# Optimization experiments

Measured on AMD Instinct MI355X. Metric: run time of the kernel, lower is better.

## Reference

```python
import jax, jax.numpy as jnp
import numpy as np

N_LAYERS = 2
NUM_BRANCHES = 3
TOPK_START = 10
TOPK_END = 3


def normalize_adj(adj):
    # symmetric degree normalization: D^-1/2 (A + I) D^-1/2
    n = adj.shape[0]
    a = jnp.clip(adj + jnp.eye(n, dtype=adj.dtype), 1e-8, jnp.inf)
    row_sum = jnp.clip(a.sum(axis=1), 1e-8, jnp.inf)
    d = jnp.clip(row_sum ** -0.5, 0.0, 100.0)
    return d[:, None] * a * d[None, :]


def setup_inputs() -> dict:
    key = jax.random.key(0)
    k1, k2 = jax.random.split(key)
    B, T, N, C = 512, 16, 22, 64
    x = jax.random.normal(k1, (B, T, N, C), dtype=jnp.float32)
    # emulate nn.Parameter init: clamp(adj,0,1)*0.01 + 0.05*I
    raw = jax.random.uniform(k2, (N, N), dtype=jnp.float32)
    adj = jnp.clip(raw, 0.0, 1.0) * 0.01 + 0.05 * jnp.eye(N, dtype=jnp.float32)
    branch_temps = jnp.ones((NUM_BRANCHES,), dtype=jnp.float32)
    fusion_logits = jnp.zeros((N_LAYERS, NUM_BRANCHES), dtype=jnp.float32)
    return {"x": x, "adj": adj, "branch_temps": branch_temps, "fusion_logits": fusion_logits}


def reference(x, adj, branch_temps, fusion_logits):
    B, T, N, C = x.shape
    # [B, T, N, C] -> [B, N, T*C]
    x0 = jnp.transpose(x, (0, 2, 1, 3)).reshape(B, N, T * C)
    A = normalize_adj(jnp.clip(adj, 0.0, 1.0))          # [N, N]
    temps = jnp.clip(branch_temps, 0.1, 10.0)           # [nb]
    eye = jnp.eye(N, dtype=x0.dtype)

    xb = x0
    for layer in range(N_LAYERS):
        K = int(TOPK_START - (TOPK_START - TOPK_END) * (layer / max(1, N_LAYERS - 1)))
        K = min(K, N)
        alpha = jax.nn.softmax(fusion_logits[layer])    # [nb]
        # cosine similarity, masked by normalized adjacency
        xn = xb / (jnp.linalg.norm(xb, axis=-1, keepdims=True) + 1e-6)
        sim = jnp.einsum('bnd,bmd->bnm', xn, xn) * A    # [B, N, N]
        # per-branch temperature + diagonal boost
        att = sim[None] / temps[:, None, None, None] + 0.1 * eye  # [nb, B, N, N]
        # annealed top-k sparsification (zeros still participate in softmax, as in torch)
        _, idx = jax.lax.top_k(att, K)                  # [nb, B, N, K]
        mask = jax.nn.one_hot(idx, N, dtype=att.dtype).sum(axis=-2)  # [nb, B, N, N]
        att = jax.nn.softmax(att * mask, axis=-1)
        y = jnp.einsum('kbnm,bmd->kbnd', att, xb)       # branch aggregation
        xb = jnp.einsum('k,kbnd->bnd', alpha, y)        # fusion
        if layer > 0:
            xb = xb + x0
        if layer < N_LAYERS - 1:
            xb = jax.nn.relu(xb)  # dropout identity in eval mode
    return xb, A
```

## Files before the change

kernel.cpp:

```cpp
#include <hip/hip_runtime.h>
#include <hip/hip_bf16.h>

#define BATCH  512
#define TT     16
#define NN     22
#define CC     64
#define DD     1024
#define NB     3
#define XS     1032
#define NTHR   512

typedef __bf16 bf16x8 __attribute__((ext_vector_type(8)));
typedef float  f32x4  __attribute__((ext_vector_type(4)));

__device__ __forceinline__ unsigned bf16rne(float x) {
  unsigned u = __float_as_uint(x);
  u += 0x7fffu + ((u >> 16) & 1u);
  return u >> 16;
}
__device__ __forceinline__ unsigned pack2(float a, float b) {
  return bf16rne(a) | (bf16rne(b) << 16);
}

__global__ __launch_bounds__(NTHR) void mbdsca_fused(
    const float* __restrict__ x,
    const float* __restrict__ adj,
    const float* __restrict__ btemps,
    const float* __restrict__ flogits,
    float* __restrict__ out)
{
  __shared__ unsigned short xs[NN][XS];
  __shared__ float As[NN][NN];
  __shared__ float Gs[NN][NN];
  __shared__ float Ws[NN][NN];
  __shared__ float attB[NB][NN][NN];
  __shared__ float norms[NN];
  __shared__ float alphas[2][NB];
  __shared__ float tvals[NB];

  const int tid = threadIdx.x;
  const int b   = blockIdx.x;
  const int lane = tid & 63;
  const int wv   = tid >> 6;

  if (tid < NN * NN) {
    int n = tid / NN, m = tid - n * NN;
    float v = adj[tid];
    v = fminf(fmaxf(v, 0.0f), 1.0f);
    if (n == m) v += 1.0f;
    v = fmaxf(v, 1e-8f);
    As[n][m] = v;
  }
  if (tid < NB) tvals[tid] = fminf(fmaxf(btemps[tid], 0.1f), 10.0f);
  __syncthreads();

  if (tid < NN) {
    float s = 0.0f;
    for (int m = 0; m < NN; ++m) s += As[tid][m];
    s = fmaxf(s, 1e-8f);
    norms[tid] = fminf(fmaxf(1.0f / sqrtf(s), 0.0f), 100.0f);
  }
  if (tid == 0) {
    for (int l = 0; l < 2; ++l) {
      float l0 = flogits[l*NB+0], l1 = flogits[l*NB+1], l2 = flogits[l*NB+2];
      float mx = fmaxf(l0, fmaxf(l1, l2));
      float e0 = __expf(l0-mx), e1 = __expf(l1-mx), e2 = __expf(l2-mx);
      float s = e0 + e1 + e2;
      alphas[l][0] = e0/s; alphas[l][1] = e1/s; alphas[l][2] = e2/s;
    }
  }
  __syncthreads();

  if (tid < NN * NN) {
    int n = tid / NN, m = tid - n * NN;
    As[n][m] = norms[n] * As[n][m] * norms[m];
  }
  #pragma unroll
  for (int j = 0; j < 11; ++j) {
    int f4  = tid + j * NTHR;
    int t   = f4 / (NN * (CC/4));
    int rem = f4 - t * (NN * (CC/4));
    int n   = rem >> 4;
    int c4  = rem & 15;
    const float4 v = *(const float4*)(&x[(size_t)b * (TT*NN*CC) + (size_t)f4 * 4]);
    uint2 p; p.x = pack2(v.x, v.y); p.y = pack2(v.z, v.w);
    *(uint2*)(&xs[n][t * CC + c4 * 4]) = p;
  }
  __syncthreads();

  for (int layer = 0; layer < 2; ++layer) {
    const int K = (layer == 0) ? 10 : 3;

    if (wv < 4) {
      const int Mt = wv >> 1, Nt = wv & 1;
      int arow = Mt * 16 + (lane & 15); if (arow > NN-1) arow = NN-1;
      int brow = Nt * 16 + (lane & 15); if (brow > NN-1) brow = NN-1;
      const int koff = (lane >> 4) * 8;
      f32x4 acc = {0.f, 0.f, 0.f, 0.f};
      #pragma unroll 4
      for (int ks = 0; ks < 32; ++ks) {
        bf16x8 a = *reinterpret_cast<const bf16x8*>(&xs[arow][ks * 32 + koff]);
        bf16x8 bb = *reinterpret_cast<const bf16x8*>(&xs[brow][ks * 32 + koff]);
        acc = __builtin_amdgcn_mfma_f32_16x16x32_bf16(a, bb, acc, 0, 0, 0);
      }
      #pragma unroll
      for (int r = 0; r < 4; ++r) {
        int row = Mt * 16 + (lane >> 4) * 4 + r;
        int col = Nt * 16 + (lane & 15);
        if (row < NN && col < NN) Gs[row][col] = acc[r];
      }
    }
    __syncthreads();

    if (tid < NN) norms[tid] = sqrtf(Gs[tid][tid]) + 1e-6f;
    __syncthreads();

    if (tid < NN * NN) {
      int n = tid / NN, m = tid - n * NN;
      Gs[n][m] = Gs[n][m] / (norms[n] * norms[m]) * As[n][m];
    }
    __syncthreads();

    for (int q = tid; q < NB * NN * NN; q += NTHR) {
      int k = q / (NN*NN), r = q - k * (NN*NN);
      int n = r / NN, m = r - n * NN;
      const float rtk = 1.0f / tvals[k];
      float v = Gs[n][m] * rtk + ((n == m) ? 0.1f : 0.0f);
      int rank = 0;
      #pragma unroll
      for (int j = 0; j < NN; ++j) {
        float vj = Gs[n][j] * rtk + ((n == j) ? 0.1f : 0.0f);
        rank += (vj > v) || (vj == v && j < m);
      }
      attB[k][n][m] = (rank < K) ? v : 0.0f;
    }
    __syncthreads();

    if (tid < NB * NN) {
      int k = tid / NN, n = tid - k * NN;
      float mx = -1e30f;
      for (int m = 0; m < NN; ++m) mx = fmaxf(mx, attB[k][n][m]);
      float s = 0.0f;
      for (int m = 0; m < NN; ++m) s += __expf(attB[k][n][m] - mx);
      float sc = alphas[layer][k] / s;
      for (int m = 0; m < NN; ++m) attB[k][n][m] = __expf(attB[k][n][m] - mx) * sc;
    }
    __syncthreads();

    if (tid < NN * NN) {
      int n = tid / NN, m = tid - n * NN;
      Ws[n][m] = attB[0][n][m] + attB[1][n][m] + attB[2][n][m];
    }
    __syncthreads();

    f32x4 acc[11];
    #pragma unroll
    for (int j = 0; j < 11; ++j) {
      const int g4 = tid + j * NTHR;
      const int n  = g4 >> 8;
      const int d4 = g4 & 255;
      f32x4 a = {0.f, 0.f, 0.f, 0.f};
      for (int m = 0; m < NN; ++m) {
        const float w = Ws[n][m];
        const uint2 u = *(const uint2*)(&xs[m][d4 * 4]);
        a[0] += w * __uint_as_float(u.x << 16);
        a[1] += w * __uint_as_float(u.x & 0xffff0000u);
        a[2] += w * __uint_as_float(u.y << 16);
        a[3] += w * __uint_as_float(u.y & 0xffff0000u);
      }
      acc[j] = a;
    }
    __syncthreads();

    if (layer == 0) {
      #pragma unroll
      for (int j = 0; j < 11; ++j) {
        const int g4 = tid + j * NTHR;
        const int n  = g4 >> 8;
        const int d4 = g4 & 255;
        f32x4 a = acc[j];
        uint2 p;
        p.x = pack2(fmaxf(a[0], 0.f), fmaxf(a[1], 0.f));
        p.y = pack2(fmaxf(a[2], 0.f), fmaxf(a[3], 0.f));
        *(uint2*)(&xs[n][d4 * 4]) = p;
      }
      __syncthreads();
    } else {
      #pragma unroll
      for (int j = 0; j < 11; ++j) {
        const int g4 = tid + j * NTHR;
        const int n  = g4 >> 8;
        const int d4 = g4 & 255;
        const float4 r = *(const float4*)(
            &x[(size_t)b * (TT*NN*CC) + (size_t)(d4 >> 4) * (NN*CC) + n * CC + (d4 & 15) * 4]);
        f32x4 a = acc[j];
        *(float4*)(&out[((size_t)b * NN + n) * DD + d4 * 4]) =
            make_float4(a[0] + r.x, a[1] + r.y, a[2] + r.z, a[3] + r.w);
      }
    }
  }

  if (b == 0 && tid < NN * NN) {
    out[(size_t)BATCH * NN * DD + tid] = As[tid / NN][tid - (tid / NN) * NN];
  }
}

extern "C" void kernel_launch(void* const* d_in, const int* in_sizes, int n_in,
                              void* d_out, int out_size, void* d_ws, size_t ws_size,
                              hipStream_t stream) {
  const float* x       = (const float*)d_in[0];
  const float* adj     = (const float*)d_in[1];
  const float* btemps  = (const float*)d_in[2];
  const float* flogits = (const float*)d_in[3];
  float* out = (float*)d_out;
  mbdsca_fused<<<BATCH, NTHR, 0, stream>>>(x, adj, btemps, flogits, out);
}
```

Before: 57.17 us.

## Move neighbor aggregation onto MFMA with hi/lo bf16 weights and split-K Gram

Replaces the per-thread scalar FMA aggregation over 22 neighbors with 16x16x32 bf16 MFMAs. The fused weight matrix is split into high and low bf16 parts so precision stays close to fp32. The Gram matrix now uses 32x32x16 MFMAs with a K-split across four waves, whose partial results are summed in shared memory. The softmax row max is computed inside the top-k rank loop, and the per-branch softmax is folded into the weight-fusion step, which removes a pass and a barrier. The trade-off is that the final output and residual accesses become scalar strided stores and loads rather than float4, and layer 0 updates xs in place per column tile.

```diff
diff --git a/kernel.cpp b/kernel.cpp
--- a/kernel.cpp
+++ b/kernel.cpp
@@ -9,9 +9,12 @@
 #define NB     3
 #define XS     1032
 #define NTHR   512
+#define WPAD   40
 
 typedef __bf16 bf16x8 __attribute__((ext_vector_type(8)));
 typedef float  f32x4  __attribute__((ext_vector_type(4)));
+typedef float  f32x16 __attribute__((ext_vector_type(16)));
+typedef short  s16x8  __attribute__((ext_vector_type(8)));
 
 __device__ __forceinline__ unsigned bf16rne(float x) {
   unsigned u = __float_as_uint(x);
@@ -31,15 +34,18 @@
 {
   __shared__ unsigned short xs[NN][XS];
   __shared__ float As[NN][NN];
-  __shared__ float Gs[NN][NN];
-  __shared__ float Ws[NN][NN];
+  __shared__ float Gp[4][NN][NN];
   __shared__ float attB[NB][NN][NN];
-  __shared__ float norms[NN];
+  __shared__ float mxs[NB][NN];
+  __shared__ float sinv[NB][NN];
+  __shared__ unsigned short Wh[32][WPAD];
+  __shared__ unsigned short Wl[32][WPAD];
+  __shared__ float dnorm[NN];
   __shared__ float alphas[2][NB];
   __shared__ float tvals[NB];
 
-  const int tid = threadIdx.x;
-  const int b   = blockIdx.x;
+  const int tid  = threadIdx.x;
+  const int b    = blockIdx.x;
   const int lane = tid & 63;
   const int wv   = tid >> 6;
 
@@ -48,17 +54,20 @@
     float v = adj[tid];
     v = fminf(fmaxf(v, 0.0f), 1.0f);
     if (n == m) v += 1.0f;
-    v = fmaxf(v, 1e-8f);
-    As[n][m] = v;
+    As[n][m] = fmaxf(v, 1e-8f);
   }
   if (tid < NB) tvals[tid] = fminf(fmaxf(btemps[tid], 0.1f), 10.0f);
+  for (int i = tid; i < 32 * WPAD / 2; i += NTHR) {
+    ((unsigned*)Wh)[i] = 0u;
+    ((unsigned*)Wl)[i] = 0u;
+  }
   __syncthreads();
 
   if (tid < NN) {
     float s = 0.0f;
     for (int m = 0; m < NN; ++m) s += As[tid][m];
     s = fmaxf(s, 1e-8f);
-    norms[tid] = fminf(fmaxf(1.0f / sqrtf(s), 0.0f), 100.0f);
+    dnorm[tid] = fminf(fmaxf(1.0f / sqrtf(s), 0.0f), 100.0f);
   }
   if (tid == 0) {
     for (int l = 0; l < 2; ++l) {
@@ -73,7 +82,7 @@
 
   if (tid < NN * NN) {
     int n = tid / NN, m = tid - n * NN;
-    As[n][m] = norms[n] * As[n][m] * norms[m];
+    As[n][m] = dnorm[n] * As[n][m] * dnorm[m];
   }
   #pragma unroll
   for (int j = 0; j < 11; ++j) {
@@ -92,32 +101,36 @@
     const int K = (layer == 0) ? 10 : 3;
 
     if (wv < 4) {
-      const int Mt = wv >> 1, Nt = wv & 1;
-      int arow = Mt * 16 + (lane & 15); if (arow > NN-1) arow = NN-1;
-      int brow = Nt * 16 + (lane & 15); if (brow > NN-1) brow = NN-1;
-      const int koff = (lane >> 4) * 8;
-      f32x4 acc = {0.f, 0.f, 0.f, 0.f};
-      #pragma unroll 4
-      for (int ks = 0; ks < 32; ++ks) {
-        bf16x8 a = *reinterpret_cast<const bf16x8*>(&xs[arow][ks * 32 + koff]);
-        bf16x8 bb = *reinterpret_cast<const bf16x8*>(&xs[brow][ks * 32 + koff]);
-        acc = __builtin_amdgcn_mfma_f32_16x16x32_bf16(a, bb, acc, 0, 0, 0);
-      }
-      #pragma unroll
-      for (int r = 0; r < 4; ++r) {
-        int row = Mt * 16 + (lane >> 4) * 4 + r;
-        int col = Nt * 16 + (lane & 15);
-        if (row < NN && col < NN) Gs[row][col] = acc[r];
-      }
-    }
-    __syncthreads();
-
-    if (tid < NN) norms[tid] = sqrtf(Gs[tid][tid]) + 1e-6f;
+      int row = lane & 31; if (row > NN-1) row = NN-1;
+      const int hi = lane >> 5;
+      f32x16 acc0 = {}, acc1 = {};
+      #pragma unroll
+      for (int s = 0; s < 16; ++s) {
+        int ks = wv * 16 + s;
+        bf16x8 a = *(const bf16x8*)(&xs[row][ks * 16 + hi * 8]);
+        if (s & 1) acc1 = __builtin_amdgcn_mfma_f32_32x32x16_bf16(a, a, acc1, 0, 0, 0);
+        else       acc0 = __builtin_amdgcn_mfma_f32_32x32x16_bf16(a, a, acc0, 0, 0, 0);
+      }
+      #pragma unroll
+      for (int r = 0; r < 16; ++r) {
+        float v = acc0[r] + acc1[r];
+        int orow = (r & 3) + 8 * (r >> 2) + 4 * hi;
+        int ocol = lane & 31;
+        if (orow < NN && ocol < NN) Gp[wv][orow][ocol] = v;
+      }
+    }
+    __syncthreads();
+
+    if (tid < NN) {
+      float gn = Gp[0][tid][tid] + Gp[1][tid][tid] + Gp[2][tid][tid] + Gp[3][tid][tid];
+      dnorm[tid] = 1.0f / (sqrtf(gn) + 1e-6f);
+    }
     __syncthreads();
 
     if (tid < NN * NN) {
       int n = tid / NN, m = tid - n * NN;
-      Gs[n][m] = Gs[n][m] / (norms[n] * norms[m]) * As[n][m];
+      float g = Gp[0][n][m] + Gp[1][n][m] + Gp[2][n][m] + Gp[3][n][m];
+      Gp[0][n][m] = g * dnorm[n] * dnorm[m] * As[n][m];
     }
     __syncthreads();
 
@@ -125,79 +138,95 @@
       int k = q / (NN*NN), r = q - k * (NN*NN);
       int n = r / NN, m = r - n * NN;
       const float rtk = 1.0f / tvals[k];
-      float v = Gs[n][m] * rtk + ((n == m) ? 0.1f : 0.0f);
-      int rank = 0;
+      float v = Gp[0][n][m] * rtk + ((n == m) ? 0.1f : 0.0f);
+      int rank = 0; float rmax = -1e30f;
       #pragma unroll
       for (int j = 0; j < NN; ++j) {
-        float vj = Gs[n][j] * rtk + ((n == j) ? 0.1f : 0.0f);
+        float vj = Gp[0][n][j] * rtk + ((n == j) ? 0.1f : 0.0f);
         rank += (vj > v) || (vj == v && j < m);
+        rmax = fmaxf(rmax, vj);
       }
       attB[k][n][m] = (rank < K) ? v : 0.0f;
+      if (m == 0) mxs[k][n] = fmaxf(rmax, 0.0f);
     }
     __syncthreads();
 
     if (tid < NB * NN) {
       int k = tid / NN, n = tid - k * NN;
-      float mx = -1e30f;
-      for (int m = 0; m < NN; ++m) mx = fmaxf(mx, attB[k][n][m]);
-      float s = 0.0f;
+      float mx = mxs[k][n], s = 0.0f;
       for (int m = 0; m < NN; ++m) s += __expf(attB[k][n][m] - mx);
-      float sc = alphas[layer][k] / s;
-      for (int m = 0; m < NN; ++m) attB[k][n][m] = __expf(attB[k][n][m] - mx) * sc;
+      sinv[k][n] = alphas[layer][k] / s;
     }
     __syncthreads();
 
     if (tid < NN * NN) {
       int n = tid / NN, m = tid - n * NN;
-      Ws[n][m] = attB[0][n][m] + attB[1][n][m] + attB[2][n][m];
-    }
-    __syncthreads();
-
-    f32x4 acc[11];
-    #pragma unroll
-    for (int j = 0; j < 11; ++j) {
-      const int g4 = tid + j * NTHR;
-      const int n  = g4 >> 8;
-      const int d4 = g4 & 255;
-      f32x4 a = {0.f, 0.f, 0.f, 0.f};
-      for (int m = 0; m < NN; ++m) {
-        const float w = Ws[n][m];
-        const uint2 u = *(const uint2*)(&xs[m][d4 * 4]);
-        a[0] += w * __uint_as_float(u.x << 16);
-        a[1] += w * __uint_as_float(u.x & 0xffff0000u);
-        a[2] += w * __uint_as_float(u.y << 16);
-        a[3] += w * __uint_as_float(u.y & 0xffff0000u);
-      }
-      acc[j] = a;
-    }
-    __syncthreads();
-
-    if (layer == 0) {
-      #pragma unroll
-      for (int j = 0; j < 11; ++j) {
-        const int g4 = tid + j * NTHR;
-        const int n  = g4 >> 8;
-        const int d4 = g4 & 255;
-        f32x4 a = acc[j];
-        uint2 p;
-        p.x = pack2(fmaxf(a[0], 0.f), fmaxf(a[1], 0.f));
-        p.y = pack2(fmaxf(a[2], 0.f), fmaxf(a[3], 0.f));
-        *(uint2*)(&xs[n][d4 * 4]) = p;
-      }
-      __syncthreads();
-    } else {
-      #pragma unroll
-      for (int j = 0; j < 11; ++j) {
-        const int g4 = tid + j * NTHR;
-        const int n  = g4 >> 8;
-        const int d4 = g4 & 255;
-        const float4 r = *(const float4*)(
-            &x[(size_t)b * (TT*NN*CC) + (size_t)(d4 >> 4) * (NN*CC) + n * CC + (d4 & 15) * 4]);
-        f32x4 a = acc[j];
-        *(float4*)(&out[((size_t)b * NN + n) * DD + d4 * 4]) =
-            make_float4(a[0] + r.x, a[1] + r.y, a[2] + r.z, a[3] + r.w);
-      }
-    }
+      float w = 0.0f;
+      #pragma unroll
+      for (int k = 0; k < NB; ++k)
+        w += __expf(attB[k][n][m] - mxs[k][n]) * sinv[k][n];
+      unsigned h = bf16rne(w);
+      float wh = __uint_as_float(h << 16);
+      Wh[n][m] = (unsigned short)h;
+      Wl[n][m] = (unsigned short)bf16rne(w - wh);
+    }
+    __syncthreads();
+
+    {
+      const int wr = lane & 15;
+      const int kg = lane >> 4;
+      bf16x8 ah0 = *(const bf16x8*)(&Wh[wr][kg * 8]);
+      bf16x8 al0 = *(const bf16x8*)(&Wl[wr][kg * 8]);
+      bf16x8 ah1 = *(const bf16x8*)(&Wh[16 + wr][kg * 8]);
+      bf16x8 al1 = *(const bf16x8*)(&Wl[16 + wr][kg * 8]);
+      #pragma unroll 2
+      for (int i = 0; i < 8; ++i) {
+        const int Nt   = wv + i * 8;
+        const int dcol = Nt * 16 + wr;
+        s16x8 bsv;
+        #pragma unroll
+        for (int j = 0; j < 8; ++j) {
+          int m  = kg * 8 + j;
+          int mc = (m < NN) ? m : 0;
+          bsv[j] = (short)xs[mc][dcol];
+        }
+        bf16x8 bfr = __builtin_bit_cast(bf16x8, bsv);
+        f32x4 y0 = {}, y1 = {};
+        y0 = __builtin_amdgcn_mfma_f32_16x16x32_bf16(al0, bfr, y0, 0, 0, 0);
+        y0 = __builtin_amdgcn_mfma_f32_16x16x32_bf16(ah0, bfr, y0, 0, 0, 0);
+        y1 = __builtin_amdgcn_mfma_f32_16x16x32_bf16(al1, bfr, y1, 0, 0, 0);
+        y1 = __builtin_amdgcn_mfma_f32_16x16x32_bf16(ah1, bfr, y1, 0, 0, 0);
+        if (layer == 0) {
+          #pragma unroll
+          for (int r = 0; r < 4; ++r) {
+            int row0 = kg * 4 + r;
+            xs[row0][dcol] = (unsigned short)bf16rne(fmaxf(y0[r], 0.0f));
+          }
+          #pragma unroll
+          for (int r = 0; r < 4; ++r) {
+            int row1 = 16 + kg * 4 + r;
+            if (row1 < NN)
+              xs[row1][dcol] = (unsigned short)bf16rne(fmaxf(y1[r], 0.0f));
+          }
+        } else {
+          const float* xres = x + (size_t)b * (TT*NN*CC);
+          const int t = dcol >> 6, c = dcol & 63;
+          float* ob = out + (size_t)b * (NN*DD) + dcol;
+          #pragma unroll
+          for (int r = 0; r < 4; ++r) {
+            int row0 = kg * 4 + r;
+            ob[row0 * DD] = y0[r] + xres[(t * NN + row0) * CC + c];
+          }
+          #pragma unroll
+          for (int r = 0; r < 4; ++r) {
+            int row1 = 16 + kg * 4 + r;
+            if (row1 < NN)
+              ob[row1 * DD] = y1[r] + xres[(t * NN + row1) * CC + c];
+          }
+        }
+      }
+    }
+    __syncthreads();
   }
 
   if (b == 0 && tid < NN * NN) {
```

Result: slower. 63.21 us (+10.6%).
